# Kernel optimization log

Measured on AMD Instinct MI355X. Metric: run time of the kernel, lower is better.

## Reference

```python
import jax, jax.numpy as jnp
import numpy as np

B, N, M, C, H, D = 1, 4096, 4096, 768, 12, 64  # batch, tgt len, src len, in_dim, heads, head_dim
SCALE = D ** -0.5


def setup_inputs() -> dict:
    key = jax.random.key(0)
    ks = jax.random.split(key, 6)
    s = 0.02
    return {
        "x": jax.random.normal(ks[0], (B, N, C), jnp.float32),
        "src": jax.random.normal(ks[1], (B, M, C), jnp.float32),
        "W_qv": jax.random.normal(ks[2], (2 * H * D, C), jnp.float32) * s,
        "W_k": jax.random.normal(ks[3], (H * D, C), jnp.float32) * s,
        "W_proj": jax.random.normal(ks[4], (C, H * D), jnp.float32) * s,
        "b_proj": jnp.zeros((C,), jnp.float32),
    }


def reference(x, src, W_qv, W_k, W_proj, b_proj):
    Bb, Nn, _ = x.shape
    Mm = src.shape[1]
    # q, v come from src; k comes from x (info flows src -> target)
    qv = (src @ W_qv.T).reshape(Bb, Mm, 2, H, D)
    q = qv[:, :, 0].transpose(0, 2, 1, 3)  # (B, H, M, D)
    v = qv[:, :, 1].transpose(0, 2, 1, 3)  # (B, H, M, D)
    k = (x @ W_k.T).reshape(Bb, Nn, H, D) * SCALE  # (B, N, H, D), pre-scaled
    # attn[b,h,n,m] = q[b,h,m,:] . k[b,n,h,:]  (torch: (q @ k).transpose(-2,-1))
    attn = jnp.einsum('bhmd,bnhd->bhnm', q, k)
    attn = jax.nn.softmax(attn, axis=-1)  # softmax over src tokens m
    y = jnp.einsum('bhnm,bhmd->bnhd', attn, v).reshape(Bb, Nn, H * D)
    return y @ W_proj.T + b_proj
```

## Files before the change

### kernel.cpp

```cpp
#include <hip/hip_runtime.h>

using f32x4 = __attribute__((ext_vector_type(4))) float;
using f32x16 = __attribute__((ext_vector_type(16))) float;
using s16x8 = __attribute__((ext_vector_type(8))) short;
using u16x4 = __attribute__((ext_vector_type(4))) unsigned short;
using u32x4 = __attribute__((ext_vector_type(4))) unsigned int;

#define AS1 __attribute__((address_space(1)))
#define AS3 __attribute__((address_space(3)))

__device__ __forceinline__ void gload16(const void* g, void* l) {
  __builtin_amdgcn_global_load_lds((const AS1 unsigned int*)g,
                                   (AS3 unsigned int*)l, 16, 0, 0);
}

__device__ __forceinline__ unsigned short f2bf(float f) {
  unsigned int u = __builtin_bit_cast(unsigned int, f);
  u += 0x7fffu + ((u >> 16) & 1u);
  return (unsigned short)(u >> 16);
}

__device__ __forceinline__ unsigned int cvtpk(float lo, float hi) {
  unsigned int w;
  asm("v_cvt_pk_bf16_f32 %0, %1, %2" : "=v"(w) : "v"(lo), "v"(hi));
  return w;
}

__device__ __forceinline__ void plswap(unsigned int& a, unsigned int& b) {
  asm("v_permlane32_swap_b32 %0, %1" : "+v"(a), "+v"(b));
}

__global__ __launch_bounds__(256) void cvt_bf16_multi(
    const float* __restrict__ i0, const float* __restrict__ i1,
    const float* __restrict__ i2, const float* __restrict__ i3,
    const float* __restrict__ i4, unsigned short* __restrict__ o0,
    unsigned short* __restrict__ o1, unsigned short* __restrict__ o2,
    unsigned short* __restrict__ o3, unsigned short* __restrict__ o4) {
  int b = blockIdx.x;
  const float* in;
  unsigned short* out;
  int base, n4;
  if (b < 3072) { in = i0; out = o0; base = b; n4 = 786432; }
  else if (b < 6144) { in = i1; out = o1; base = b - 3072; n4 = 786432; }
  else if (b < 7296) { in = i2; out = o2; base = b - 6144; n4 = 294912; }
  else if (b < 7872) { in = i3; out = o3; base = b - 7296; n4 = 147456; }
  else { in = i4; out = o4; base = b - 7872; n4 = 147456; }
  int i = base * 256 + threadIdx.x;
  if (i >= n4) return;
  f32x4 v = ((const f32x4*)in)[i];
  u16x4 r;
#pragma unroll
  for (int j = 0; j < 4; ++j) r[j] = f2bf(v[j]);
  ((u16x4*)out)[i] = r;
}

__global__ __launch_bounds__(256) void gemm_proj(
    const unsigned short* __restrict__ srcb, const unsigned short* __restrict__ wqvb,
    const unsigned short* __restrict__ xb, const unsigned short* __restrict__ wkb,
    unsigned short* __restrict__ qbuf, unsigned short* __restrict__ vtbuf,
    unsigned short* __restrict__ kbuf) {
  __shared__ __align__(16) unsigned short As[128 * 64];
  __shared__ __align__(16) unsigned short Bs[128 * 64];
  const bool isqv = blockIdx.y < 12;
  const unsigned short* A = isqv ? srcb : xb;
  const unsigned short* B = isqv ? wqvb : wkb;
  const int n0 = (isqv ? blockIdx.y : (blockIdx.y - 12)) * 128;
  const int m0 = blockIdx.x * 128;
  const int t = threadIdx.x;
  const int lane = t & 63;
  const int wid = t >> 6;
  const int wr = wid >> 1, wc = wid & 1;
  const int fr = lane & 15, fq = lane >> 4;

  f32x4 acc[4][4];
#pragma unroll
  for (int i = 0; i < 4; ++i)
#pragma unroll
    for (int j = 0; j < 4; ++j) acc[i][j] = (f32x4){0.f, 0.f, 0.f, 0.f};

  const char* Ab = (const char*)A;
  const char* Bb = (const char*)B;

  for (int k0 = 0; k0 < 768; k0 += 64) {
#pragma unroll
    for (int p = 0; p < 4; ++p) {
      int idx = p * 256 + t;
      int row = idx >> 3;
      int scb = ((idx & 7) << 4) ^ ((row & 7) << 4);
      char* dstA = (char*)As + (p * 256 + (wid << 6)) * 16;
      char* dstB = (char*)Bs + (p * 256 + (wid << 6)) * 16;
      gload16(Ab + (size_t)(m0 + row) * 1536 + (size_t)k0 * 2 + scb, dstA);
      gload16(Bb + (size_t)(n0 + row) * 1536 + (size_t)k0 * 2 + scb, dstB);
    }
    __syncthreads();

    s16x8 af[4][2], bfr[4][2];
#pragma unroll
    for (int mi = 0; mi < 4; ++mi)
#pragma unroll
      for (int kk = 0; kk < 2; ++kk) {
        int row = wr * 64 + mi * 16 + fr;
        int cb = (kk * 64 + (fq << 4)) ^ ((row & 7) << 4);
        af[mi][kk] = *(const s16x8*)((const char*)As + row * 128 + cb);
      }
#pragma unroll
    for (int ni = 0; ni < 4; ++ni)
#pragma unroll
      for (int kk = 0; kk < 2; ++kk) {
        int row = wc * 64 + ni * 16 + fr;
        int cb = (kk * 64 + (fq << 4)) ^ ((row & 7) << 4);
        bfr[ni][kk] = *(const s16x8*)((const char*)Bs + row * 128 + cb);
      }
    __builtin_amdgcn_s_setprio(1);
#pragma unroll
    for (int kk = 0; kk < 2; ++kk)
#pragma unroll
      for (int mi = 0; mi < 4; ++mi)
#pragma unroll
        for (int ni = 0; ni < 4; ++ni)
          acc[mi][ni] = __builtin_amdgcn_mfma_f32_16x16x32_bf16(
              af[mi][kk], bfr[ni][kk], acc[mi][ni], 0, 0, 0);
    __builtin_amdgcn_s_setprio(0);
    __syncthreads();
  }

#pragma unroll
  for (int mi = 0; mi < 4; ++mi) {
#pragma unroll
    for (int ni = 0; ni < 4; ++ni) {
      int row0 = m0 + wr * 64 + mi * 16 + (fq << 2);
      int col = n0 + wc * 64 + ni * 16 + fr;
      if (isqv) {
        if (n0 < 768) {
#pragma unroll
          for (int j = 0; j < 4; ++j)
            qbuf[(size_t)(row0 + j) * 768 + col] = f2bf(acc[mi][ni][j]);
        } else {
          u16x4 pk;
#pragma unroll
          for (int j = 0; j < 4; ++j) pk[j] = f2bf(acc[mi][ni][j]);
          *(u16x4*)(vtbuf + (size_t)(col - 768) * 4096 + row0) = pk;
        }
      } else {
#pragma unroll
        for (int j = 0; j < 4; ++j)
          kbuf[(size_t)(row0 + j) * 768 + col] = f2bf(acc[mi][ni][j] * 0.18033688f);
      }
    }
  }
}

__global__ __launch_bounds__(256) void gemm_out(
    const unsigned short* __restrict__ A, const unsigned short* __restrict__ B,
    float* __restrict__ outp, const float* __restrict__ bias) {
  __shared__ __align__(16) unsigned short As[128 * 64];
  __shared__ __align__(16) unsigned short Bs[128 * 64];
  const int t = threadIdx.x;
  const int lane = t & 63;
  const int wid = t >> 6;
  const int wr = wid >> 1, wc = wid & 1;
  const int m0 = blockIdx.x * 128, n0 = blockIdx.y * 128;
  const int fr = lane & 15, fq = lane >> 4;

  f32x4 acc[4][4];
#pragma unroll
  for (int i = 0; i < 4; ++i)
#pragma unroll
    for (int j = 0; j < 4; ++j) acc[i][j] = (f32x4){0.f, 0.f, 0.f, 0.f};

  for (int k0 = 0; k0 < 768; k0 += 64) {
#pragma unroll
    for (int p = 0; p < 4; ++p) {
      int idx = p * 256 + t;
      int row = idx >> 3;
      int scb = ((idx & 7) << 4) ^ ((row & 7) << 4);
      char* dstA = (char*)As + (p * 256 + (wid << 6)) * 16;
      char* dstB = (char*)Bs + (p * 256 + (wid << 6)) * 16;
      gload16((const char*)A + (size_t)(m0 + row) * 1536 + (size_t)k0 * 2 + scb, dstA);
      gload16((const char*)B + (size_t)(n0 + row) * 1536 + (size_t)k0 * 2 + scb, dstB);
    }
    __syncthreads();

    s16x8 af[4][2], bfr[4][2];
#pragma unroll
    for (int mi = 0; mi < 4; ++mi)
#pragma unroll
      for (int kk = 0; kk < 2; ++kk) {
        int row = wr * 64 + mi * 16 + fr;
        int cb = (kk * 64 + (fq << 4)) ^ ((row & 7) << 4);
        af[mi][kk] = *(const s16x8*)((const char*)As + row * 128 + cb);
      }
#pragma unroll
    for (int ni = 0; ni < 4; ++ni)
#pragma unroll
      for (int kk = 0; kk < 2; ++kk) {
        int row = wc * 64 + ni * 16 + fr;
        int cb = (kk * 64 + (fq << 4)) ^ ((row & 7) << 4);
        bfr[ni][kk] = *(const s16x8*)((const char*)Bs + row * 128 + cb);
      }
    __builtin_amdgcn_s_setprio(1);
#pragma unroll
    for (int kk = 0; kk < 2; ++kk)
#pragma unroll
      for (int mi = 0; mi < 4; ++mi)
#pragma unroll
        for (int ni = 0; ni < 4; ++ni)
          acc[mi][ni] = __builtin_amdgcn_mfma_f32_16x16x32_bf16(
              af[mi][kk], bfr[ni][kk], acc[mi][ni], 0, 0, 0);
    __builtin_amdgcn_s_setprio(0);
    __syncthreads();
  }

#pragma unroll
  for (int mi = 0; mi < 4; ++mi) {
#pragma unroll
    for (int ni = 0; ni < 4; ++ni) {
      int row0 = m0 + wr * 64 + mi * 16 + (fq << 2);
      int col = n0 + wc * 64 + ni * 16 + fr;
      float bv = bias[col];
#pragma unroll
      for (int j = 0; j < 4; ++j)
        outp[(size_t)(row0 + j) * 768 + col] = acc[mi][ni][j] + bv;
    }
  }
}

__global__ __launch_bounds__(256, 4) void attn_kernel(
    const unsigned short* __restrict__ Qk, const unsigned short* __restrict__ Kq,
    const unsigned short* __restrict__ Vt, float* __restrict__ Po0,
    float* __restrict__ PoR, float* __restrict__ Pl) {
  __shared__ __align__(16) unsigned short Ks[2][64 * 64];
  __shared__ __align__(16) unsigned short Vs[2][64 * 64];
  const int t = threadIdx.x, lane = t & 63, wid = t >> 6;
  const int half = lane >> 5, l31 = lane & 31;

  int bid = blockIdx.x;
  int f = (bid & 7) * 192 + (bid >> 3);
  const int h = f >> 7;
  const int rem = f & 127;
  const int n0 = (rem >> 2) * 128;
  const int sp = rem & 3;
  const int mbase = sp * 1024;

  s16x8 qf[4];
  {
    const size_t qrow = n0 + wid * 32 + l31;
#pragma unroll
    for (int kc = 0; kc < 4; ++kc)
      qf[kc] = *(const s16x8*)(Qk + qrow * 768 + h * 64 + kc * 16 + half * 8);
  }

  f32x16 o[2];
#pragma unroll
  for (int dt = 0; dt < 2; ++dt)
#pragma unroll
    for (int r = 0; r < 16; ++r) o[dt][r] = 0.f;
  float lsum = 0.f;

  const int rswz = (l31 & 7) << 4;
  const int rbase = l31 * 128;
  int coff[4];
#pragma unroll
  for (int kc = 0; kc < 4; ++kc)
    coff[kc] = (kc * 32 + half * 16) ^ rswz;

  auto stage = [&](int buf, int m0) {
#pragma unroll
    for (int p = 0; p < 2; ++p) {
      int idx = p * 256 + t;
      int row = idx >> 3;
      int scb = ((idx & 7) << 4) ^ ((row & 7) << 4);
      char* dk = (char*)Ks[buf] + (p * 256 + (wid << 6)) * 16;
      char* dv = (char*)Vs[buf] + (p * 256 + (wid << 6)) * 16;
      gload16((const char*)Kq + (size_t)(m0 + row) * 1536 + h * 128 + scb, dk);
      gload16((const char*)Vt + (size_t)(h * 64 + row) * 8192 + (size_t)m0 * 2 + scb, dv);
    }
  };

  stage(0, mbase);
  __syncthreads();

  for (int it = 0; it < 16; ++it) {
    const int buf = it & 1;
    if (it < 15) stage(buf ^ 1, mbase + (it + 1) * 64);

    const char* Ksb = (const char*)Ks[buf];
    const char* Vsb = (const char*)Vs[buf];

    f32x16 s[2];
#pragma unroll
    for (int mt = 0; mt < 2; ++mt)
#pragma unroll
      for (int r = 0; r < 16; ++r) s[mt][r] = 0.f;
    __builtin_amdgcn_s_setprio(1);
#pragma unroll
    for (int mt = 0; mt < 2; ++mt)
#pragma unroll
      for (int kc = 0; kc < 4; ++kc) {
        s16x8 kf = *(const s16x8*)(Ksb + mt * 4096 + rbase + coff[kc]);
        s[mt] = __builtin_amdgcn_mfma_f32_32x32x16_bf16(kf, qf[kc], s[mt], 0, 0, 0);
      }
    __builtin_amdgcn_s_setprio(0);

#pragma unroll
    for (int mt = 0; mt < 2; ++mt)
#pragma unroll
      for (int r = 0; r < 16; ++r) {
        s[mt][r] = __builtin_exp2f(s[mt][r]);
        lsum += s[mt][r];
      }

    s16x8 pfrag[4];
#pragma unroll
    for (int mt = 0; mt < 2; ++mt) {
      unsigned int w[8];
#pragma unroll
      for (int i = 0; i < 8; ++i) w[i] = cvtpk(s[mt][2 * i], s[mt][2 * i + 1]);
      plswap(w[0], w[2]);
      plswap(w[1], w[3]);
      plswap(w[4], w[6]);
      plswap(w[5], w[7]);
      u32x4 f0, f1;
      f0[0] = w[0]; f0[1] = w[1]; f0[2] = w[2]; f0[3] = w[3];
      f1[0] = w[4]; f1[1] = w[5]; f1[2] = w[6]; f1[3] = w[7];
      pfrag[2 * mt] = __builtin_bit_cast(s16x8, f0);
      pfrag[2 * mt + 1] = __builtin_bit_cast(s16x8, f1);
    }

    __builtin_amdgcn_s_setprio(1);
#pragma unroll
    for (int dt = 0; dt < 2; ++dt)
#pragma unroll
      for (int kc = 0; kc < 4; ++kc) {
        s16x8 vf = *(const s16x8*)(Vsb + dt * 4096 + rbase + coff[kc]);
        o[dt] = __builtin_amdgcn_mfma_f32_32x32x16_bf16(vf, pfrag[kc], o[dt], 0, 0, 0);
      }
    __builtin_amdgcn_s_setprio(0);
    __syncthreads();
  }

  lsum += __shfl_xor(lsum, 32);
  float* Po = (sp == 0) ? Po0 : (PoR + (size_t)(sp - 1) * 3145728);
  const size_t n = n0 + wid * 32 + l31;
  if (!half) Pl[sp * 49152 + n * 12 + h] = lsum;
#pragma unroll
  for (int dt = 0; dt < 2; ++dt)
#pragma unroll
    for (int g = 0; g < 4; ++g) {
      f32x4 v;
#pragma unroll
      for (int e = 0; e < 4; ++e) v[e] = o[dt][4 * g + e];
      int d = dt * 32 + 8 * g + 4 * half;
      *(f32x4*)(Po + n * 768 + h * 64 + d) = v;
    }
}

__global__ __launch_bounds__(256) void attn_combine(
    const float* __restrict__ Po0, const float* __restrict__ PoR,
    const float* __restrict__ Pl, unsigned short* __restrict__ Y) {
  int idx = blockIdx.x * 256 + threadIdx.x;
  int row = idx / 192;
  int c4 = idx - row * 192;
  int col = c4 * 4;
  int h = col >> 6;
  float l = Pl[(size_t)row * 12 + h] + Pl[49152 + (size_t)row * 12 + h] +
            Pl[2 * 49152 + (size_t)row * 12 + h] +
            Pl[3 * 49152 + (size_t)row * 12 + h];
  float inv = 1.0f / l;
  size_t off = (size_t)row * 768 + col;
  f32x4 a = *(const f32x4*)(Po0 + off);
  f32x4 b = *(const f32x4*)(PoR + off);
  f32x4 c = *(const f32x4*)(PoR + 3145728 + off);
  f32x4 d = *(const f32x4*)(PoR + 2 * 3145728 + off);
  u16x4 r;
#pragma unroll
  for (int e = 0; e < 4; ++e) r[e] = f2bf((a[e] + b[e] + c[e] + d[e]) * inv);
  *(u16x4*)(Y + (size_t)row * 768 + col) = r;
}

extern "C" void kernel_launch(void* const* d_in, const int* in_sizes, int n_in,
                              void* d_out, int out_size, void* d_ws,
                              size_t ws_size, hipStream_t stream) {
  const float* x = (const float*)d_in[0];
  const float* src = (const float*)d_in[1];
  const float* Wqv = (const float*)d_in[2];
  const float* Wk = (const float*)d_in[3];
  const float* Wp = (const float*)d_in[4];
  const float* bp = (const float*)d_in[5];
  float* out = (float*)d_out;

  char* ws = (char*)d_ws;
  unsigned short* srcb = (unsigned short*)(ws + 0);
  unsigned short* xb   = (unsigned short*)(ws + 6291456);
  unsigned short* wqvb = (unsigned short*)(ws + 12582912);
  unsigned short* wkb  = (unsigned short*)(ws + 14942208);
  unsigned short* wpb  = (unsigned short*)(ws + 16121856);
  unsigned short* qbuf = (unsigned short*)(ws + 17301504);
  unsigned short* vtbuf= (unsigned short*)(ws + 23592960);
  unsigned short* kbuf = (unsigned short*)(ws + 29884416);
  unsigned short* ybuf = (unsigned short*)(ws + 36175872);
  float* part0 = (float*)(ws + 0);
  float* lsums = (float*)(ws + 12582912);
  float* partR = (float*)(ws + 42467328);

  cvt_bf16_multi<<<8448, 256, 0, stream>>>(src, x, Wqv, Wk, Wp, srcb, xb, wqvb,
                                           wkb, wpb);

  gemm_proj<<<dim3(32, 18), 256, 0, stream>>>(srcb, wqvb, xb, wkb, qbuf, vtbuf,
                                              kbuf);
  attn_kernel<<<1536, 256, 0, stream>>>(kbuf, qbuf, vtbuf, part0, partR, lsums);
  attn_combine<<<3072, 256, 0, stream>>>(part0, partR, lsums, ybuf);
  gemm_out<<<dim3(32, 6), 256, 0, stream>>>(ybuf, wpb, out, bp);
}
```

Baseline: 152.7 us.

## Single-buffer attention K/V staging and raise occupancy target to six blocks

The attention kernel drops double-buffered K/V shared-memory staging for a single buffer, halving its LDS footprint. Launch bounds rise from 4 to 6 blocks per CU so more workgroups can be resident and hide load latency by switching between them instead of overlapping in software. Staging addresses are precomputed once and advanced by pointer increments. The cost is that each iteration now waits on its own loads before computing, and the tighter register budget may cause spills.

```diff
diff --git a/kernel.cpp b/kernel.cpp
--- a/kernel.cpp
+++ b/kernel.cpp
@@ -225,12 +225,12 @@
   }
 }
 
-__global__ __launch_bounds__(256, 4) void attn_kernel(
+__global__ __launch_bounds__(256, 6) void attn_kernel(
     const unsigned short* __restrict__ Qk, const unsigned short* __restrict__ Kq,
     const unsigned short* __restrict__ Vt, float* __restrict__ Po0,
     float* __restrict__ PoR, float* __restrict__ Pl) {
-  __shared__ __align__(16) unsigned short Ks[2][64 * 64];
-  __shared__ __align__(16) unsigned short Vs[2][64 * 64];
+  __shared__ __align__(16) unsigned short Ks[64 * 64];
+  __shared__ __align__(16) unsigned short Vs[64 * 64];
   const int t = threadIdx.x, lane = t & 63, wid = t >> 6;
   const int half = lane >> 5, l31 = lane & 31;
 
@@ -264,28 +264,23 @@
   for (int kc = 0; kc < 4; ++kc)
     coff[kc] = (kc * 32 + half * 16) ^ rswz;
 
-  auto stage = [&](int buf, int m0) {
+  const int srow = t >> 3;
+  const int scb = ((t & 7) << 4) ^ ((srow & 7) << 4);
+  const char* kp = (const char*)Kq + (size_t)(mbase + srow) * 1536 + h * 128 + scb;
+  const char* vp = (const char*)Vt + (size_t)(h * 64 + srow) * 8192 +
+                   (size_t)mbase * 2 + scb;
+  char* kd = (char*)Ks + (wid << 6) * 16;
+  char* vd = (char*)Vs + (wid << 6) * 16;
+
+  for (int it = 0; it < 16; ++it) {
 #pragma unroll
     for (int p = 0; p < 2; ++p) {
-      int idx = p * 256 + t;
-      int row = idx >> 3;
-      int scb = ((idx & 7) << 4) ^ ((row & 7) << 4);
-      char* dk = (char*)Ks[buf] + (p * 256 + (wid << 6)) * 16;
-      char* dv = (char*)Vs[buf] + (p * 256 + (wid << 6)) * 16;
-      gload16((const char*)Kq + (size_t)(m0 + row) * 1536 + h * 128 + scb, dk);
-      gload16((const char*)Vt + (size_t)(h * 64 + row) * 8192 + (size_t)m0 * 2 + scb, dv);
-    }
-  };
-
-  stage(0, mbase);
-  __syncthreads();
-
-  for (int it = 0; it < 16; ++it) {
-    const int buf = it & 1;
-    if (it < 15) stage(buf ^ 1, mbase + (it + 1) * 64);
-
-    const char* Ksb = (const char*)Ks[buf];
-    const char* Vsb = (const char*)Vs[buf];
+      gload16(kp + (size_t)p * 49152, kd + p * 4096);
+      gload16(vp + (size_t)p * 262144, vd + p * 4096);
+    }
+    kp += 98304;
+    vp += 128;
+    __syncthreads();
 
     f32x16 s[2];
 #pragma unroll
@@ -297,7 +292,7 @@
     for (int mt = 0; mt < 2; ++mt)
 #pragma unroll
       for (int kc = 0; kc < 4; ++kc) {
-        s16x8 kf = *(const s16x8*)(Ksb + mt * 4096 + rbase + coff[kc]);
+        s16x8 kf = *(const s16x8*)((const char*)Ks + mt * 4096 + rbase + coff[kc]);
         s[mt] = __builtin_amdgcn_mfma_f32_32x32x16_bf16(kf, qf[kc], s[mt], 0, 0, 0);
       }
     __builtin_amdgcn_s_setprio(0);
@@ -332,7 +327,7 @@
     for (int dt = 0; dt < 2; ++dt)
 #pragma unroll
       for (int kc = 0; kc < 4; ++kc) {
-        s16x8 vf = *(const s16x8*)(Vsb + dt * 4096 + rbase + coff[kc]);
+        s16x8 vf = *(const s16x8*)((const char*)Vs + dt * 4096 + rbase + coff[kc]);
         o[dt] = __builtin_amdgcn_mfma_f32_32x32x16_bf16(vf, pfrag[kc], o[dt], 0, 0, 0);
       }
     __builtin_amdgcn_s_setprio(0);
```

New measurement: 450.2 us. +194.8%, slower.
